# Optimization experiments

Hardware: AMD Instinct MI355X
Metric: run time of the kernel (lower is better)

## Reference

```python
import jax, jax.numpy as jnp
import numpy as np
from jax import lax

DEPTH = 2            # number of CSWinBlocks in BasicLayerV2
B, H0, W0, C = 8, 56, 56, 256
NUM_HEADS = 8
SS = 7               # split_size
MLP_RATIO = 4


def setup_inputs() -> dict:
    key = jax.random.key(0)
    ks = jax.random.split(key, 8)
    C2 = C // 2
    s = 0.02
    return dict(
        x=jax.random.normal(ks[0], (B, H0 * W0, C), jnp.float32),
        ln1_g=jnp.ones((DEPTH, C), jnp.float32),
        ln1_b=jnp.zeros((DEPTH, C), jnp.float32),
        qkv_w=jax.random.normal(ks[1], (DEPTH, C, 3 * C), jnp.float32) * s,
        qkv_b=jnp.zeros((DEPTH, 3 * C), jnp.float32),
        lepe_w0=jax.random.normal(ks[2], (DEPTH, C2, 1, 3, 3), jnp.float32) * s,
        lepe_b0=jnp.zeros((DEPTH, C2), jnp.float32),
        lepe_w1=jax.random.normal(ks[3], (DEPTH, C2, 1, 3, 3), jnp.float32) * s,
        lepe_b1=jnp.zeros((DEPTH, C2), jnp.float32),
        proj_w=jax.random.normal(ks[4], (DEPTH, C, C), jnp.float32) * s,
        proj_b=jnp.zeros((DEPTH, C), jnp.float32),
        ln2_g=jnp.ones((DEPTH, C), jnp.float32),
        ln2_b=jnp.zeros((DEPTH, C), jnp.float32),
        fc1_w=jax.random.normal(ks[5], (DEPTH, C, MLP_RATIO * C), jnp.float32) * s,
        fc1_b=jnp.zeros((DEPTH, MLP_RATIO * C), jnp.float32),
        fc2_w=jax.random.normal(ks[6], (DEPTH, MLP_RATIO * C, C), jnp.float32) * s,
        fc2_b=jnp.zeros((DEPTH, C), jnp.float32),
        H=H0, W=W0,
    )


def _ln(x, g, b):
    m = x.mean(-1, keepdims=True)
    v = ((x - m) ** 2).mean(-1, keepdims=True)
    return (x - m) * lax.rsqrt(v + 1e-5) * g + b


def _win_part(x, hs, ws):
    # [B,H,W,C] -> [nW, hs*ws, C]  (matches img2windows)
    Bx, H, W, Cx = x.shape
    x = x.reshape(Bx, H // hs, hs, W // ws, ws, Cx).transpose(0, 1, 3, 2, 4, 5)
    return x.reshape(-1, hs * ws, Cx)


def _win_merge(w, hs, ws, H, W):
    # [nW, hs*ws, C] -> [B,H,W,C]  (matches windows2img)
    Cx = w.shape[-1]
    Bx = w.shape[0] // ((H // hs) * (W // ws))
    x = w.reshape(Bx, H // hs, W // ws, hs, ws, Cx).transpose(0, 1, 3, 2, 4, 5)
    return x.reshape(Bx, H, W, Cx)


def _lepe_attn(q, k, v, hs, ws, H, W, heads, cw, cb):
    # q,k,v: [B, H*W, Cb]; cross-shaped window attention + depthwise-conv LePE
    Bx, L, Cb = q.shape
    hd = Cb // heads
    scale = hd ** -0.5
    win = hs * ws
    qw = _win_part(q.reshape(Bx, H, W, Cb), hs, ws).reshape(-1, win, heads, hd).transpose(0, 2, 1, 3)
    kw = _win_part(k.reshape(Bx, H, W, Cb), hs, ws).reshape(-1, win, heads, hd).transpose(0, 2, 1, 3)
    # v as per-window images [nW, Cb, hs, ws]
    vi = v.reshape(Bx, H // hs, hs, W // ws, ws, Cb).transpose(0, 1, 3, 5, 2, 4).reshape(-1, Cb, hs, ws)
    lepe = lax.conv_general_dilated(
        vi, cw, (1, 1), 'SAME',
        dimension_numbers=('NCHW', 'OIHW', 'NCHW'),
        feature_group_count=Cb) + cb[None, :, None, None]
    lepe = lepe.reshape(-1, heads, hd, win).transpose(0, 1, 3, 2)
    vw = vi.reshape(-1, heads, hd, win).transpose(0, 1, 3, 2)
    attn = jax.nn.softmax(jnp.einsum('whqd,whkd->whqk', qw * scale, kw), axis=-1)
    o = jnp.einsum('whqk,whkd->whqd', attn, vw) + lepe
    o = o.transpose(0, 2, 1, 3).reshape(-1, win, Cb)
    return _win_merge(o, hs, ws, H, W).reshape(Bx, H * W, Cb)


def reference(x, ln1_g, ln1_b, qkv_w, qkv_b, lepe_w0, lepe_b0, lepe_w1, lepe_b1,
              proj_w, proj_b, ln2_g, ln2_b, fc1_w, fc1_b, fc2_w, fc2_b, H, W):
    Bx, L, Cx = x.shape
    C2 = Cx // 2
    h2 = NUM_HEADS // 2
    for l in range(ln1_g.shape[0]):
        img = _ln(x, ln1_g[l], ln1_b[l])
        qkv = (img @ qkv_w[l] + qkv_b[l]).reshape(Bx, L, 3, Cx)
        q, k, v = qkv[:, :, 0], qkv[:, :, 1], qkv[:, :, 2]
        # branch 0: full-height strips (H_sp=H, W_sp=SS); branch 1: full-width strips
        x1 = _lepe_attn(q[..., :C2], k[..., :C2], v[..., :C2], H, SS, H, W, h2, lepe_w0[l], lepe_b0[l])
        x2 = _lepe_attn(q[..., C2:], k[..., C2:], v[..., C2:], SS, W, H, W, h2, lepe_w1[l], lepe_b1[l])
        att = jnp.concatenate([x1, x2], axis=-1) @ proj_w[l] + proj_b[l]
        x = x + att
        y = _ln(x, ln2_g[l], ln2_b[l])
        y = jax.nn.gelu(y @ fc1_w[l] + fc1_b[l], approximate=False) @ fc2_w[l] + fc2_b[l]
        x = x + y
    return x
```

## Files before the change

### kernel.cpp

```cpp
#include <hip/hip_runtime.h>
#include <hip/hip_bf16.h>

using bf16 = __hip_bfloat16;
typedef __attribute__((ext_vector_type(8))) short short8v;
typedef __attribute__((ext_vector_type(4))) float f32x4;

#define MFMA16(a,b,c) __builtin_amdgcn_mfma_f32_16x16x32_bf16((a),(b),(c),0,0,0)

static constexpr int Bn = 8;
static constexpr int Ll = 56 * 56;
static constexpr int Mrows = Bn * Ll;

__device__ __forceinline__ void gload16(const void* g, void* l) {
  __builtin_amdgcn_global_load_lds(
      (const __attribute__((address_space(1))) void*)g,
      (__attribute__((address_space(3))) void*)l, 16, 0, 0);
}

__device__ __forceinline__ unsigned pack2(float a, float b) {
  unsigned ua = (unsigned)__bfloat16_as_ushort(__float2bfloat16(a));
  unsigned ub = (unsigned)__bfloat16_as_ushort(__float2bfloat16(b));
  return ua | (ub << 16);
}

__global__ __launch_bounds__(256) void ln_kernel(const float* __restrict__ x,
    const float* __restrict__ g, const float* __restrict__ b,
    bf16* __restrict__ out) {
  int lane = threadIdx.x & 63;
  int row = blockIdx.x * 4 + (threadIdx.x >> 6);
  const float4 v = *reinterpret_cast<const float4*>(x + (size_t)row * 256 + lane * 4);
  float s = v.x + v.y + v.z + v.w;
  float sq = v.x * v.x + v.y * v.y + v.z * v.z + v.w * v.w;
#pragma unroll
  for (int m = 1; m < 64; m <<= 1) {
    s += __shfl_xor(s, m, 64);
    sq += __shfl_xor(sq, m, 64);
  }
  float mean = s * (1.0f / 256.0f);
  float rstd = rsqrtf(sq * (1.0f / 256.0f) - mean * mean + 1e-5f);
  const float4 gg = *reinterpret_cast<const float4*>(g + lane * 4);
  const float4 bb = *reinterpret_cast<const float4*>(b + lane * 4);
  bf16 o[4];
  o[0] = __float2bfloat16((v.x - mean) * rstd * gg.x + bb.x);
  o[1] = __float2bfloat16((v.y - mean) * rstd * gg.y + bb.y);
  o[2] = __float2bfloat16((v.z - mean) * rstd * gg.z + bb.z);
  o[3] = __float2bfloat16((v.w - mean) * rstd * gg.w + bb.w);
  *reinterpret_cast<uint2*>(out + (size_t)row * 256 + lane * 4) =
      *reinterpret_cast<const uint2*>(o);
}

struct WTDesc { const float* in; bf16* out; int K; int N; int bx0; };
struct WTArgs { WTDesc d[8]; };
__global__ __launch_bounds__(256) void wtrans_all(WTArgs a) {
  __shared__ float t[32][33];
  int gb = blockIdx.x;
  int i = 0;
#pragma unroll
  for (int j = 1; j < 8; j++) if (gb >= a.d[j].bx0) i = j;
  const float* in = a.d[i].in;
  bf16* out = a.d[i].out;
  int K = a.d[i].K, N = a.d[i].N;
  int local = gb - a.d[i].bx0;
  int nbk = K >> 5;
  int bx = local % nbk, by = local / nbk;
  int tx = threadIdx.x & 31, ty = threadIdx.x >> 5;
  int k0 = bx * 32, n0 = by * 32;
#pragma unroll
  for (int q = 0; q < 4; q++)
    t[ty + q * 8][tx] = in[(size_t)(k0 + ty + q * 8) * N + n0 + tx];
  __syncthreads();
#pragma unroll
  for (int q = 0; q < 4; q++)
    out[(size_t)(n0 + ty + q * 8) * K + k0 + tx] = __float2bfloat16(t[tx][ty + q * 8]);
}

template <int EPI, int BM>
__global__ __launch_bounds__(256) void gemm_kernel(
    const bf16* __restrict__ A, const bf16* __restrict__ Bt,
    const float* __restrict__ bias, const float* __restrict__ resid,
    void* __restrict__ outp, int M, int N, int K) {
  constexpr int NI = (BM == 128) ? 4 : 2;
  __shared__ bf16 Al[2][BM * 64];
  __shared__ bf16 Bl[2][128 * 64];
  int tid = threadIdx.x, lane = tid & 63, wid = tid >> 6;
  int brow = blockIdx.y, bcol = blockIdx.x;
  int wrow = (BM == 128) ? (wid >> 1) : 0;
  int wcol = (BM == 128) ? (wid & 1) : wid;
  f32x4 acc[4][NI];
#pragma unroll
  for (int i = 0; i < 4; i++)
#pragma unroll
    for (int j = 0; j < NI; j++) acc[i][j] = f32x4{0.f, 0.f, 0.f, 0.f};

  int r8 = lane >> 3;
  int c8 = ((lane & 7) ^ r8) * 8;
  const bf16* ga0 = A + (size_t)(brow * BM + r8) * K + c8;
  const bf16* gb0 = Bt + (size_t)(bcol * 128 + r8) * K + c8;

  auto stage = [&](bf16* Ad, bf16* Bd, int kt) {
#pragma unroll
    for (int c = 0; c < BM / 32; c++) {
      int chunk = c * 4 + wid;
      gload16(ga0 + (size_t)chunk * 8 * K + kt, Ad + chunk * 512);
    }
#pragma unroll
    for (int c = 0; c < 4; c++) {
      int chunk = c * 4 + wid;
      gload16(gb0 + (size_t)chunk * 8 * K + kt, Bd + chunk * 512);
    }
  };

  stage(Al[0], Bl[0], 0);
  asm volatile("s_waitcnt vmcnt(0)" ::: "memory");
  __builtin_amdgcn_s_barrier();

  int lg = lane >> 4, ql = lane & 15, qx = ql & 7;
  int nk = K >> 6;
  int cur = 0;
  for (int t = 0; t < nk; t++) {
    bf16* Ac = Al[cur];
    bf16* Bc = Bl[cur];
    if (t + 1 < nk) stage(Al[cur ^ 1], Bl[cur ^ 1], (t + 1) * 64);
#pragma unroll
    for (int kk = 0; kk < 64; kk += 32) {
      int slot = ((kk >> 3) + lg) ^ qx;
      short8v av[4], bv[NI];
#pragma unroll
      for (int mi = 0; mi < 4; mi++)
        av[mi] = *reinterpret_cast<const short8v*>(
            &Ac[(wrow * 64 + mi * 16 + ql) * 64 + slot * 8]);
#pragma unroll
      for (int ni = 0; ni < NI; ni++)
        bv[ni] = *reinterpret_cast<const short8v*>(
            &Bc[(wcol * (NI * 16) + ni * 16 + ql) * 64 + slot * 8]);
#pragma unroll
      for (int mi = 0; mi < 4; mi++)
#pragma unroll
        for (int ni = 0; ni < NI; ni++)
          acc[mi][ni] = MFMA16(av[mi], bv[ni], acc[mi][ni]);
    }
    asm volatile("s_waitcnt vmcnt(0)" ::: "memory");
    __builtin_amdgcn_s_barrier();
    cur ^= 1;
  }

  int rowb = brow * BM + wrow * 64 + ((lane >> 4) * 4);
  int colb = bcol * 128 + wcol * (NI * 16) + (lane & 15);
#pragma unroll
  for (int ni = 0; ni < NI; ni++) {
    int col = colb + ni * 16;
    float bvl = bias[col];
#pragma unroll
    for (int mi = 0; mi < 4; mi++) {
#pragma unroll
      for (int r = 0; r < 4; r++) {
        int row = rowb + mi * 16 + r;
        float v = acc[mi][ni][r] + bvl;
        if (EPI == 0) {
          ((bf16*)outp)[(size_t)row * N + col] = __float2bfloat16(v);
        } else if (EPI == 1) {
          float gv = 0.5f * v * (1.0f + erff(v * 0.70710678118654752f));
          ((bf16*)outp)[(size_t)row * N + col] = __float2bfloat16(gv);
        } else {
          float* o = (float*)outp + (size_t)row * N + col;
          *o += v;
        }
      }
    }
  }
}

template <int RES>
__global__ __launch_bounds__(256) void gemm_ln_kernel(
    const bf16* __restrict__ A, const bf16* __restrict__ Bt,
    const float* __restrict__ bias, const float* __restrict__ resid,
    float* __restrict__ xout, const float* __restrict__ g,
    const float* __restrict__ b, bf16* __restrict__ lnout, int K) {
  __shared__ bf16 Al[2][64 * 64];
  __shared__ bf16 Bl[2][256 * 64];
  int tid = threadIdx.x, lane = tid & 63, wid = tid >> 6;
  int brow = blockIdx.x;
  f32x4 acc[4][4];
#pragma unroll
  for (int i = 0; i < 4; i++)
#pragma unroll
    for (int j = 0; j < 4; j++) acc[i][j] = f32x4{0.f, 0.f, 0.f, 0.f};

  int r8 = lane >> 3;
  int c8 = ((lane & 7) ^ r8) * 8;
  const bf16* ga0 = A + (size_t)(brow * 64 + r8) * K + c8;
  const bf16* gb0 = Bt + (size_t)r8 * K + c8;

  auto stage = [&](bf16* Ad, bf16* Bd, int kt) {
#pragma unroll
    for (int c = 0; c < 2; c++) {
      int chunk = c * 4 + wid;
      gload16(ga0 + (size_t)chunk * 8 * K + kt, Ad + chunk * 512);
    }
#pragma unroll
    for (int c = 0; c < 8; c++) {
      int chunk = c * 4 + wid;
      gload16(gb0 + (size_t)chunk * 8 * K + kt, Bd + chunk * 512);
    }
  };

  stage(Al[0], Bl[0], 0);
  asm volatile("s_waitcnt vmcnt(0)" ::: "memory");
  __builtin_amdgcn_s_barrier();

  int lg = lane >> 4, ql = lane & 15, qx = ql & 7;
  int nk = K >> 6;
  int cur = 0;
  for (int t = 0; t < nk; t++) {
    bf16* Ac = Al[cur];
    bf16* Bc = Bl[cur];
    if (t + 1 < nk) stage(Al[cur ^ 1], Bl[cur ^ 1], (t + 1) * 64);
#pragma unroll
    for (int kk = 0; kk < 64; kk += 32) {
      int slot = ((kk >> 3) + lg) ^ qx;
      short8v av[4], bv[4];
#pragma unroll
      for (int mi = 0; mi < 4; mi++)
        av[mi] = *reinterpret_cast<const short8v*>(
            &Ac[(mi * 16 + ql) * 64 + slot * 8]);
#pragma unroll
      for (int ni = 0; ni < 4; ni++)
        bv[ni] = *reinterpret_cast<const short8v*>(
            &Bc[(wid * 64 + ni * 16 + ql) * 64 + slot * 8]);
#pragma unroll
      for (int mi = 0; mi < 4; mi++)
#pragma unroll
        for (int ni = 0; ni < 4; ni++)
          acc[mi][ni] = MFMA16(av[mi], bv[ni], acc[mi][ni]);
    }
    asm volatile("s_waitcnt vmcnt(0)" ::: "memory");
    __builtin_amdgcn_s_barrier();
    cur ^= 1;
  }

  float xv[4][4][4];
  float psum[4][4], psq[4][4];
#pragma unroll
  for (int mi = 0; mi < 4; mi++)
#pragma unroll
    for (int r = 0; r < 4; r++) { psum[mi][r] = 0.f; psq[mi][r] = 0.f; }

#pragma unroll
  for (int ni = 0; ni < 4; ni++) {
    int col = wid * 64 + ni * 16 + ql;
    float bvl = bias[col];
#pragma unroll
    for (int mi = 0; mi < 4; mi++) {
#pragma unroll
      for (int r = 0; r < 4; r++) {
        size_t row = (size_t)brow * 64 + mi * 16 + lg * 4 + r;
        float base = RES ? resid[row * 256 + col] : xout[row * 256 + col];
        float v = base + acc[mi][ni][r] + bvl;
        xv[mi][ni][r] = v;
        psum[mi][r] += v;
        psq[mi][r] += v * v;
      }
    }
  }
#pragma unroll
  for (int mi = 0; mi < 4; mi++)
#pragma unroll
    for (int r = 0; r < 4; r++) {
#pragma unroll
      for (int m = 1; m < 16; m <<= 1) {
        psum[mi][r] += __shfl_xor(psum[mi][r], m, 64);
        psq[mi][r] += __shfl_xor(psq[mi][r], m, 64);
      }
    }
  float* red = (float*)&Al[0][0];
  float* red2 = red + 512;
  if (ql == 0) {
#pragma unroll
    for (int mi = 0; mi < 4; mi++)
#pragma unroll
      for (int r = 0; r < 4; r++) {
        int lr = mi * 16 + lg * 4 + r;
        red[lr * 8 + wid] = psum[mi][r];
        red[lr * 8 + 4 + wid] = psq[mi][r];
      }
  }
  __syncthreads();
  if (tid < 64) {
    float s = red[tid * 8] + red[tid * 8 + 1] + red[tid * 8 + 2] + red[tid * 8 + 3];
    float q = red[tid * 8 + 4] + red[tid * 8 + 5] + red[tid * 8 + 6] + red[tid * 8 + 7];
    float mean = s * (1.0f / 256.0f);
    float rstd = rsqrtf(q * (1.0f / 256.0f) - mean * mean + 1e-5f);
    red2[tid * 2] = mean;
    red2[tid * 2 + 1] = rstd;
  }
  __syncthreads();
#pragma unroll
  for (int mi = 0; mi < 4; mi++) {
#pragma unroll
    for (int r = 0; r < 4; r++) {
      int lr = mi * 16 + lg * 4 + r;
      float mean = red2[lr * 2], rstd = red2[lr * 2 + 1];
      size_t row = (size_t)brow * 64 + lr;
#pragma unroll
      for (int ni = 0; ni < 4; ni++) {
        int col = wid * 64 + ni * 16 + ql;
        float v = xv[mi][ni][r];
        xout[row * 256 + col] = v;
        lnout[row * 256 + col] =
            __float2bfloat16((v - mean) * rstd * g[col] + b[col]);
      }
    }
  }
}

__global__ __launch_bounds__(512, 2) void attn_kernel(const bf16* __restrict__ qkv,
    bf16* __restrict__ att,
    const float* __restrict__ lw0, const float* __restrict__ lb0,
    const float* __restrict__ lw1, const float* __restrict__ lb1) {
  __shared__ bf16 Kl[400 * 40];
  __shared__ bf16 Vt[32 * 456];
  __shared__ float wl[288];
  __shared__ float bl[32];

  int tid = threadIdx.x, lane = tid & 63, wid = tid >> 6;
  int wh = blockIdx.x;
  int branch = wh >> 8;
  int head = wh & 3;
  int widx = (wh >> 2) & 63;
  int bimg = widx >> 3, g7 = widx & 7;
  int cb = branch * 128 + head * 32;
  size_t base = (size_t)bimg * Ll * 768;

  auto tok2l = [&](int t) -> int {
    if (branch == 0) { int d = t / 7;  return d * 56 + g7 * 7 + (t - d * 7); }
    else             { int d = t / 56; return (g7 * 7 + d) * 56 + (t - d * 56); }
  };

  for (int idx = tid; idx < 392 * 4; idx += 512) {
    int t = idx >> 2, dq = (idx & 3) * 8;
    size_t go = base + (size_t)tok2l(t) * 768 + cb + dq;
    uint4 kv = *reinterpret_cast<const uint4*>(qkv + go + 256);
    *reinterpret_cast<uint4*>(&Kl[t * 40 + dq]) = kv;
    uint4 vv = *reinterpret_cast<const uint4*>(qkv + go + 512);
    const bf16* pv = reinterpret_cast<const bf16*>(&vv);
    int swz = (idx & 3) << 3;
#pragma unroll
    for (int j = 0; j < 8; j++) Vt[(dq + j) * 456 + (t ^ swz)] = pv[j];
  }
  bf16 z16 = __float2bfloat16(0.0f);
  if (tid < 320) Kl[392 * 40 + tid] = z16;
  for (int idx = tid; idx < 1024; idx += 512) {
    int d = idx >> 5, c = 392 + (idx & 31);
    Vt[d * 456 + (c ^ (((d >> 3) & 3) << 3))] = z16;
  }
  {
    const float* wsel = (branch ? lw1 : lw0) + head * 288;
    const float* bsel = (branch ? lb1 : lb0) + head * 32;
    if (tid < 288) wl[tid] = wsel[tid];
    else if (tid < 320) bl[tid - 288] = bsel[tid - 288];
  }
  __syncthreads();

  const float c1 = 0.25506275154111575f;
  const f32x4 zz = {0.f, 0.f, 0.f, 0.f};
  int lg = lane >> 4;
  int ql = lane & 15;
  int sw0 = ((ql >> 3) & 1) << 3;
  int sw1 = sw0 + 16;

  auto epilogue = [&](int mt, float lsum, const f32x4& oA, const f32x4& oB) {
    int qo = mt * 16 + ql;
    if (qo >= 392) return;
    float inv = 1.0f / lsum;
    int wb_ = branch ? 56 : 7;
    int hb_ = branch ? 7 : 56;
    int lh = branch ? (qo / 56) : (qo / 7);
    int lw_ = qo - lh * wb_;
    float lep[8];
#pragma unroll
    for (int i = 0; i < 8; i++) lep[i] = bl[(i >> 2) * 16 + 4 * lg + (i & 3)];
#pragma unroll
    for (int dy = -1; dy <= 1; dy++) {
#pragma unroll
      for (int dx = -1; dx <= 1; dx++) {
        if ((unsigned)(lh + dy) < (unsigned)hb_ &&
            (unsigned)(lw_ + dx) < (unsigned)wb_) {
          int nt = qo + dy * wb_ + dx;
          int tap = (dy + 1) * 3 + (dx + 1);
#pragma unroll
          for (int i = 0; i < 8; i++) {
            int d = (i >> 2) * 16 + 4 * lg + (i & 3);
            lep[i] += wl[d * 9 + tap] *
                __bfloat162float(Vt[d * 456 + (nt ^ (((d >> 3) & 3) << 3))]);
          }
        }
      }
    }
    size_t ob = ((size_t)bimg * Ll + tok2l(qo)) * 256 + cb + 4 * lg;
    bf16 o4[4];
#pragma unroll
    for (int r = 0; r < 4; r++) o4[r] = __float2bfloat16(oA[r] * inv + lep[r]);
    *reinterpret_cast<uint2*>(att + ob) = *reinterpret_cast<const uint2*>(o4);
#pragma unroll
    for (int r = 0; r < 4; r++) o4[r] = __float2bfloat16(oB[r] * inv + lep[4 + r]);
    *reinterpret_cast<uint2*>(att + ob + 16) = *reinterpret_cast<const uint2*>(o4);
  };

  int mt0 = -1, mt1 = -1;
  if (blockIdx.y == 0) {
    if (wid < 6) { mt0 = 2 * wid; mt1 = 2 * wid + 1; }
    else if (wid == 6) { mt0 = 12; }
  } else {
    if (wid < 6) { mt0 = 13 + 2 * wid; mt1 = 14 + 2 * wid; }
  }

  if (mt0 >= 0) {
    int qr0 = mt0 * 16 + ql; if (qr0 > 391) qr0 = 391;
    int mtb = (mt1 >= 0) ? mt1 : mt0;
    int qr1 = mtb * 16 + ql; if (qr1 > 391) qr1 = 391;
    short8v qf0 = *reinterpret_cast<const short8v*>(
        qkv + base + (size_t)tok2l(qr0) * 768 + cb + lg * 8);
    short8v qf1 = *reinterpret_cast<const short8v*>(
        qkv + base + (size_t)tok2l(qr1) * 768 + cb + lg * 8);

    float ls0 = 0.f, ls1 = 0.f;
    f32x4 o00 = zz, o01 = zz, o10 = zz, o11 = zz;

#pragma unroll
    for (int c = 0; c < 13; c++) {
      short8v kf0 = *reinterpret_cast<const short8v*>(
          &Kl[(c * 32 + ql) * 40 + lg * 8]);
      f32x4 sA0, sB0, sA1, sB1;
      __builtin_amdgcn_s_setprio(1);
      sA0 = MFMA16(kf0, qf0, zz);
      sB0 = MFMA16(kf0, qf1, zz);
      __builtin_amdgcn_s_setprio(0);
      if (c < 12) {
        short8v kf1 = *reinterpret_cast<const short8v*>(
            &Kl[(c * 32 + 16 + ql) * 40 + lg * 8]);
        __builtin_amdgcn_s_setprio(1);
        sA1 = MFMA16(kf1, qf0, zz);
        sB1 = MFMA16(kf1, qf1, zz);
        __builtin_amdgcn_s_setprio(0);
      }
      float pA0[4], pA1[4], pB0[4], pB1[4];
#pragma unroll
      for (int r = 0; r < 4; r++) {
        if (c == 12) {
          pA0[r] = (lg < 2) ? exp2f(sA0[r] * c1) : 0.f;
          pB0[r] = (lg < 2) ? exp2f(sB0[r] * c1) : 0.f;
          pA1[r] = 0.f; pB1[r] = 0.f;
        } else {
          pA0[r] = exp2f(sA0[r] * c1);
          pA1[r] = exp2f(sA1[r] * c1);
          pB0[r] = exp2f(sB0[r] * c1);
          pB1[r] = exp2f(sB1[r] * c1);
        }
        ls0 += pA0[r] + pA1[r];
        ls1 += pB0[r] + pB1[r];
      }
      uint4 pwA, pwB;
      pwA.x = pack2(pA0[0], pA0[1]); pwA.y = pack2(pA0[2], pA0[3]);
      pwA.z = pack2(pA1[0], pA1[1]); pwA.w = pack2(pA1[2], pA1[3]);
      pwB.x = pack2(pB0[0], pB0[1]); pwB.y = pack2(pB0[2], pB0[3]);
      pwB.z = pack2(pB1[0], pB1[1]); pwB.w = pack2(pB1[2], pB1[3]);
      short8v pfA = *reinterpret_cast<const short8v*>(&pwA);
      short8v pfB = *reinterpret_cast<const short8v*>(&pwB);

      int col0 = c * 32 + 4 * lg;
      uint2 a0 = *reinterpret_cast<const uint2*>(&Vt[ql * 456 + (col0 ^ sw0)]);
      uint2 a1 = *reinterpret_cast<const uint2*>(&Vt[ql * 456 + ((col0 + 16) ^ sw0)]);
      uint2 b0 = *reinterpret_cast<const uint2*>(&Vt[(16 + ql) * 456 + (col0 ^ sw1)]);
      uint2 b1 = *reinterpret_cast<const uint2*>(&Vt[(16 + ql) * 456 + ((col0 + 16) ^ sw1)]);
      uint4 va = {a0.x, a0.y, a1.x, a1.y};
      uint4 vb = {b0.x, b0.y, b1.x, b1.y};
      short8v vf0 = *reinterpret_cast<const short8v*>(&va);
      short8v vf1 = *reinterpret_cast<const short8v*>(&vb);
      __builtin_amdgcn_s_setprio(1);
      o00 = MFMA16(vf0, pfA, o00);
      o01 = MFMA16(vf1, pfA, o01);
      o10 = MFMA16(vf0, pfB, o10);
      o11 = MFMA16(vf1, pfB, o11);
      __builtin_amdgcn_s_setprio(0);
    }

    ls0 += __shfl_xor(ls0, 16, 64);
    ls0 += __shfl_xor(ls0, 32, 64);
    ls1 += __shfl_xor(ls1, 16, 64);
    ls1 += __shfl_xor(ls1, 32, 64);

    epilogue(mt0, ls0, o00, o01);
    if (mt1 >= 0) epilogue(mt1, ls1, o10, o11);
  }
}

extern "C" void kernel_launch(void* const* d_in, const int* in_sizes, int n_in,
                              void* d_out, int out_size, void* d_ws, size_t ws_size,
                              hipStream_t stream) {
  const float* x_in    = (const float*)d_in[0];
  const float* ln1_g   = (const float*)d_in[1];
  const float* ln1_b   = (const float*)d_in[2];
  const float* qkv_w   = (const float*)d_in[3];
  const float* qkv_b   = (const float*)d_in[4];
  const float* lepe_w0 = (const float*)d_in[5];
  const float* lepe_b0 = (const float*)d_in[6];
  const float* lepe_w1 = (const float*)d_in[7];
  const float* lepe_b1 = (const float*)d_in[8];
  const float* proj_w  = (const float*)d_in[9];
  const float* proj_b  = (const float*)d_in[10];
  const float* ln2_g   = (const float*)d_in[11];
  const float* ln2_b   = (const float*)d_in[12];
  const float* fc1_w   = (const float*)d_in[13];
  const float* fc1_b   = (const float*)d_in[14];
  const float* fc2_w   = (const float*)d_in[15];
  const float* fc2_b   = (const float*)d_in[16];
  float* xf = (float*)d_out;

  char* ws = (char*)d_ws;
  bf16* wT   = (bf16*)ws;
  bf16* bufA = (bf16*)(ws + 3145728);
  bf16* imgB = (bf16*)(ws + 3145728 + 51380224);
  bf16* attB = (bf16*)(ws + 3145728 + 51380224 + 12845056);

  {
    WTArgs a;
    int off = 0;
    for (int l = 0; l < 2; l++) {
      bf16* qkvT = wT + (size_t)l * 786432;
      WTDesc d[4] = {
        {qkv_w + l * 196608, qkvT,          256, 768,  0},
        {proj_w + l * 65536, qkvT + 196608, 256, 256,  0},
        {fc1_w + l * 262144, qkvT + 262144, 256, 1024, 0},
        {fc2_w + l * 262144, qkvT + 524288, 1024, 256, 0},
      };
      for (int j = 0; j < 4; j++) {
        d[j].bx0 = off;
        off += (d[j].K >> 5) * (d[j].N >> 5);
        a.d[l * 4 + j] = d[j];
      }
    }
    wtrans_all<<<off, 256, 0, stream>>>(a);
  }

  for (int l = 0; l < 2; l++) {
    bf16* qkvT = wT + (size_t)l * 786432;
    bf16* projT = qkvT + 196608;
    bf16* fc1T  = qkvT + 262144;
    bf16* fc2T  = qkvT + 524288;

    if (l == 0)
      ln_kernel<<<Mrows / 4, 256, 0, stream>>>(x_in, ln1_g, ln1_b, imgB);

    gemm_kernel<0, 128><<<dim3(6, 196), 256, 0, stream>>>(imgB, qkvT, qkv_b + l * 768,
                                                          nullptr, bufA, Mrows, 768, 256);
    attn_kernel<<<dim3(512, 2), 512, 0, stream>>>(bufA, attB,
                                                  lepe_w0 + l * 1152, lepe_b0 + l * 128,
                                                  lepe_w1 + l * 1152, lepe_b1 + l * 128);
    if (l == 0) {
      gemm_ln_kernel<1><<<392, 256, 0, stream>>>(attB, projT, proj_b, x_in, xf,
                                                 ln2_g, ln2_b, imgB, 256);
    } else {
      gemm_ln_kernel<0><<<392, 256, 0, stream>>>(attB, projT, proj_b + 256, xf, xf,
                                                 ln2_g + 256, ln2_b + 256, imgB, 256);
    }
    gemm_kernel<1, 128><<<dim3(8, 196), 256, 0, stream>>>(imgB, fc1T, fc1_b + l * 1024,
                                                          nullptr, bufA, Mrows, 1024, 256);
    if (l == 0) {
      gemm_ln_kernel<0><<<392, 256, 0, stream>>>(bufA, fc2T, fc2_b, xf, xf,
                                                 ln1_g + 256, ln1_b + 256, imgB, 1024);
    } else {
      gemm_kernel<2, 64><<<dim3(2, 392), 256, 0, stream>>>(bufA, fc2T, fc2_b + 256,
                                                           nullptr, xf, Mrows, 256, 1024);
    }
  }
}
```

Measured before the change: 385.4 us.

## Shrink attention LDS, async-load K, fold softmax scale into QKV GEMM

Removes the padding on the K and V-transpose shared-memory tiles and raises the attention kernel's launch bound from 2 to 6 blocks per CU, so more blocks can be resident. K tiles are now copied straight from global memory into LDS with global_load_lds instead of going through registers. The softmax scale (including log2e) is applied to Q in a new QKV GEMM epilogue, which removes a multiply per score in the attention loop. Dropping the padding can bring back LDS bank conflicts on K reads, and storing pre-scaled Q in bf16 slightly changes rounding.

```diff
diff --git a/kernel.cpp b/kernel.cpp
--- a/kernel.cpp
+++ b/kernel.cpp
@@ -161,9 +161,12 @@
         } else if (EPI == 1) {
           float gv = 0.5f * v * (1.0f + erff(v * 0.70710678118654752f));
           ((bf16*)outp)[(size_t)row * N + col] = __float2bfloat16(gv);
-        } else {
+        } else if (EPI == 2) {
           float* o = (float*)outp + (size_t)row * N + col;
           *o += v;
+        } else {
+          float sc = (col < 256) ? 0.25506275154111575f : 1.0f;
+          ((bf16*)outp)[(size_t)row * N + col] = __float2bfloat16(v * sc);
         }
       }
     }
@@ -222,7 +225,7 @@
 #pragma unroll
       for (int mi = 0; mi < 4; mi++)
         av[mi] = *reinterpret_cast<const short8v*>(
-            &Ac[(mi * 16 + ql) * 64 + slot * 8]);
+            &Al[cur][(mi * 16 + ql) * 64 + slot * 8]);
 #pragma unroll
       for (int ni = 0; ni < 4; ni++)
         bv[ni] = *reinterpret_cast<const short8v*>(
@@ -313,12 +316,12 @@
   }
 }
 
-__global__ __launch_bounds__(512, 2) void attn_kernel(const bf16* __restrict__ qkv,
+__global__ __launch_bounds__(512, 6) void attn_kernel(const bf16* __restrict__ qkv,
     bf16* __restrict__ att,
     const float* __restrict__ lw0, const float* __restrict__ lb0,
     const float* __restrict__ lw1, const float* __restrict__ lb1) {
-  __shared__ bf16 Kl[400 * 40];
-  __shared__ bf16 Vt[32 * 456];
+  __shared__ bf16 Kl[400 * 32];
+  __shared__ bf16 Vt[32 * 416];
   __shared__ float wl[288];
   __shared__ float bl[32];
 
@@ -336,22 +339,28 @@
     else             { int d = t / 56; return (g7 * 7 + d) * 56 + (t - d * 56); }
   };
 
-  for (int idx = tid; idx < 392 * 4; idx += 512) {
+#pragma unroll
+  for (int it = 0; it < 4; it++) {
+    int chunk = it * 512 + tid;
+    if (chunk < 1568) {
+      int t = chunk >> 2, dc = (chunk & 3) * 8;
+      gload16(qkv + base + (size_t)tok2l(t) * 768 + 256 + cb + dc,
+              Kl + (size_t)(it * 512 + wid * 64) * 8);
+    }
+  }
+  for (int idx = tid; idx < 1568; idx += 512) {
     int t = idx >> 2, dq = (idx & 3) * 8;
-    size_t go = base + (size_t)tok2l(t) * 768 + cb + dq;
-    uint4 kv = *reinterpret_cast<const uint4*>(qkv + go + 256);
-    *reinterpret_cast<uint4*>(&Kl[t * 40 + dq]) = kv;
-    uint4 vv = *reinterpret_cast<const uint4*>(qkv + go + 512);
+    uint4 vv = *reinterpret_cast<const uint4*>(
+        qkv + base + (size_t)tok2l(t) * 768 + 512 + cb + dq);
     const bf16* pv = reinterpret_cast<const bf16*>(&vv);
     int swz = (idx & 3) << 3;
 #pragma unroll
-    for (int j = 0; j < 8; j++) Vt[(dq + j) * 456 + (t ^ swz)] = pv[j];
+    for (int j = 0; j < 8; j++) Vt[(dq + j) * 416 + (t ^ swz)] = pv[j];
   }
   bf16 z16 = __float2bfloat16(0.0f);
-  if (tid < 320) Kl[392 * 40 + tid] = z16;
-  for (int idx = tid; idx < 1024; idx += 512) {
-    int d = idx >> 5, c = 392 + (idx & 31);
-    Vt[d * 456 + (c ^ (((d >> 3) & 3) << 3))] = z16;
+  for (int idx = tid; idx < 768; idx += 512) {
+    int d = idx / 24, c = 392 + (idx - (idx / 24) * 24);
+    Vt[d * 416 + (c ^ (((d >> 3) & 3) << 3))] = z16;
   }
   {
     const float* wsel = (branch ? lw1 : lw0) + head * 288;
@@ -361,7 +370,6 @@
   }
   __syncthreads();
 
-  const float c1 = 0.25506275154111575f;
   const f32x4 zz = {0.f, 0.f, 0.f, 0.f};
   int lg = lane >> 4;
   int ql = lane & 15;
@@ -391,7 +399,7 @@
           for (int i = 0; i < 8; i++) {
             int d = (i >> 2) * 16 + 4 * lg + (i & 3);
             lep[i] += wl[d * 9 + tap] *
-                __bfloat162float(Vt[d * 456 + (nt ^ (((d >> 3) & 3) << 3))]);
+                __bfloat162float(Vt[d * 416 + (nt ^ (((d >> 3) & 3) << 3))]);
           }
         }
       }
@@ -429,7 +437,7 @@
 #pragma unroll
     for (int c = 0; c < 13; c++) {
       short8v kf0 = *reinterpret_cast<const short8v*>(
-          &Kl[(c * 32 + ql) * 40 + lg * 8]);
+          &Kl[(c * 32 + ql) * 32 + lg * 8]);
       f32x4 sA0, sB0, sA1, sB1;
       __builtin_amdgcn_s_setprio(1);
       sA0 = MFMA16(kf0, qf0, zz);
@@ -437,7 +445,7 @@
       __builtin_amdgcn_s_setprio(0);
       if (c < 12) {
         short8v kf1 = *reinterpret_cast<const short8v*>(
-            &Kl[(c * 32 + 16 + ql) * 40 + lg * 8]);
+            &Kl[(c * 32 + 16 + ql) * 32 + lg * 8]);
         __builtin_amdgcn_s_setprio(1);
         sA1 = MFMA16(kf1, qf0, zz);
         sB1 = MFMA16(kf1, qf1, zz);
@@ -447,14 +455,14 @@
 #pragma unroll
       for (int r = 0; r < 4; r++) {
         if (c == 12) {
-          pA0[r] = (lg < 2) ? exp2f(sA0[r] * c1) : 0.f;
-          pB0[r] = (lg < 2) ? exp2f(sB0[r] * c1) : 0.f;
+          pA0[r] = (lg < 2) ? exp2f(sA0[r]) : 0.f;
+          pB0[r] = (lg < 2) ? exp2f(sB0[r]) : 0.f;
           pA1[r] = 0.f; pB1[r] = 0.f;
         } else {
-          pA0[r] = exp2f(sA0[r] * c1);
-          pA1[r] = exp2f(sA1[r] * c1);
-          pB0[r] = exp2f(sB0[r] * c1);
-          pB1[r] = exp2f(sB1[r] * c1);
+          pA0[r] = exp2f(sA0[r]);
+          pA1[r] = exp2f(sA1[r]);
+          pB0[r] = exp2f(sB0[r]);
+          pB1[r] = exp2f(sB1[r]);
         }
         ls0 += pA0[r] + pA1[r];
         ls1 += pB0[r] + pB1[r];
@@ -468,10 +476,10 @@
       short8v pfB = *reinterpret_cast<const short8v*>(&pwB);
 
       int col0 = c * 32 + 4 * lg;
-      uint2 a0 = *reinterpret_cast<const uint2*>(&Vt[ql * 456 + (col0 ^ sw0)]);
-      uint2 a1 = *reinterpret_cast<const uint2*>(&Vt[ql * 456 + ((col0 + 16) ^ sw0)]);
-      uint2 b0 = *reinterpret_cast<const uint2*>(&Vt[(16 + ql) * 456 + (col0 ^ sw1)]);
-      uint2 b1 = *reinterpret_cast<const uint2*>(&Vt[(16 + ql) * 456 + ((col0 + 16) ^ sw1)]);
+      uint2 a0 = *reinterpret_cast<const uint2*>(&Vt[ql * 416 + (col0 ^ sw0)]);
+      uint2 a1 = *reinterpret_cast<const uint2*>(&Vt[ql * 416 + ((col0 + 16) ^ sw0)]);
+      uint2 b0 = *reinterpret_cast<const uint2*>(&Vt[(16 + ql) * 416 + (col0 ^ sw1)]);
+      uint2 b1 = *reinterpret_cast<const uint2*>(&Vt[(16 + ql) * 416 + ((col0 + 16) ^ sw1)]);
       uint4 va = {a0.x, a0.y, a1.x, a1.y};
       uint4 vb = {b0.x, b0.y, b1.x, b1.y};
       short8v vf0 = *reinterpret_cast<const short8v*>(&va);
@@ -551,7 +559,7 @@
     if (l == 0)
       ln_kernel<<<Mrows / 4, 256, 0, stream>>>(x_in, ln1_g, ln1_b, imgB);
 
-    gemm_kernel<0, 128><<<dim3(6, 196), 256, 0, stream>>>(imgB, qkvT, qkv_b + l * 768,
+    gemm_kernel<4, 128><<<dim3(6, 196), 256, 0, stream>>>(imgB, qkvT, qkv_b + l * 768,
                                                           nullptr, bufA, Mrows, 768, 256);
     attn_kernel<<<dim3(512, 2), 512, 0, stream>>>(bufA, attB,
                                                   lepe_w0 + l * 1152, lepe_b0 + l * 128,
```

New measurement: 381.4 us. No clear change (-1.0%).
